# Performance work log

Measured on AMD Instinct MI355X. Metric: run time of the kernel, lower is better.

The kernel has to match this reference:

```python
import jax, jax.numpy as jnp
import numpy as np

FI_BIT, FI_GROUP = 8, 64
FW_BIT, FW_GROUP = 8, 64


def quantize_bfp(x, bit, group):
    """Block-floating-point quantize: groups of `group` elems along the last dim
    share the exponent of the group max; mantissas are rounded to `bit` bits."""
    shp = x.shape
    xg = x.reshape(shp[:-1] + (shp[-1] // group, group))
    maxabs = jnp.max(jnp.abs(xg), axis=-1, keepdims=True)
    e = jnp.floor(jnp.log2(jnp.maximum(maxabs, jnp.asarray(1e-38, x.dtype))))
    step = jnp.exp2(e - (bit - 1))  # quantization step for shared exponent e
    qmax = 2 ** (bit - 1) - 1
    q = jnp.clip(jnp.round(xg / step), -(qmax + 1), qmax) * step
    q = jnp.where(maxabs == 0, jnp.zeros_like(q), q)
    return q.reshape(shp)


def setup_inputs() -> dict:
    key = jax.random.key(0)
    k1, k2, k3 = jax.random.split(key, 3)
    N, IN, OUT = 4096, 4096, 4096
    x = jax.random.normal(k1, (N, IN), dtype=jnp.float32)
    # weight/bias initialized uniform(-0.1, 0.1) as in the torch module
    weight = jax.random.uniform(k2, (OUT, IN), dtype=jnp.float32, minval=-0.1, maxval=0.1)
    bias = jax.random.uniform(k3, (OUT,), dtype=jnp.float32, minval=-0.1, maxval=0.1)
    return {"x": x, "weight": weight, "bias": bias}


def reference(x, weight, bias):
    xq = quantize_bfp(x, FI_BIT, FI_GROUP)          # [N, IN]
    wq = quantize_bfp(weight, FW_BIT, FW_GROUP)     # [OUT, IN]
    out = jnp.einsum('ni,oi->no', xq, wq)
    # Faithful to the original forward: F.linear adds bias once, then the
    # explicit `output += bias` adds it a second time.
    out = out + 2.0 * bias[None, :]
    return out
```

## Files before the change

### kernel.cpp

```cpp
#include <hip/hip_runtime.h>
#include <stdint.h>

typedef __bf16 bf16_t;
typedef __attribute__((ext_vector_type(8))) __bf16 bf16x8;
typedef __attribute__((ext_vector_type(4))) float f32x4;

#define NDIM 4096

__global__ __launch_bounds__(256) void quant_bfp(const float* __restrict__ in0,
                                                 bf16_t* __restrict__ out0,
                                                 const float* __restrict__ in1,
                                                 bf16_t* __restrict__ out1) {
    const float* in = blockIdx.y ? in1 : in0;
    bf16_t* out     = blockIdx.y ? out1 : out0;
    const int t = blockIdx.x * 256 + threadIdx.x;
    float4 a = ((const float4*)in)[2 * t];
    float4 b = ((const float4*)in)[2 * t + 1];
    float m = fmaxf(fmaxf(fmaxf(fabsf(a.x), fabsf(a.y)), fmaxf(fabsf(a.z), fabsf(a.w))),
                    fmaxf(fmaxf(fabsf(b.x), fabsf(b.y)), fmaxf(fabsf(b.z), fabsf(b.w))));
    m = fmaxf(m, __shfl_xor(m, 1));
    m = fmaxf(m, __shfl_xor(m, 2));
    m = fmaxf(m, __shfl_xor(m, 4));
    const int e = (int)((__float_as_uint(m) >> 23) & 0xFF) - 127;
    float step = __uint_as_float((uint32_t)(e + 120) << 23);
    float inv  = __uint_as_float((uint32_t)(134 - e) << 23);
    if (m == 0.0f) { step = 0.0f; inv = 0.0f; }
    float q[8] = {a.x, a.y, a.z, a.w, b.x, b.y, b.z, b.w};
    union { bf16_t h[8]; uint4 u; } o;
#pragma unroll
    for (int i = 0; i < 8; ++i)
        o.h[i] = (bf16_t)(fminf(fmaxf(rintf(q[i] * inv), -128.0f), 127.0f) * step);
    ((uint4*)out)[t] = o.u;
}

__device__ __forceinline__ void g2l16(const bf16_t* g, void* l) {
    __builtin_amdgcn_global_load_lds(
        (__attribute__((address_space(1))) void*)g,
        (__attribute__((address_space(3))) void*)l, 16, 0, 0);
}

__global__ __launch_bounds__(256) void gemm_bfp(const bf16_t* __restrict__ A,
                                                const bf16_t* __restrict__ B,
                                                const float* __restrict__ bias,
                                                float* __restrict__ C) {
    __shared__ bf16_t sA[128 * 64];
    __shared__ bf16_t sB[128 * 64];

    const int tid  = threadIdx.x;
    const int wave = tid >> 6;
    const int lane = tid & 63;

    const int p  = blockIdx.y * 32 + blockIdx.x;
    const int bn = ((p & 7) << 2) | ((p >> 3) & 3);
    const int bm = p >> 5;

    const int m_wave = (wave >> 1) * 64;
    const int n_wave = (wave & 1) * 64;

    const int srow = tid >> 3;
    const int swz  = (((tid & 7) ^ (srow & 7)) * 8);

    const bf16_t* pA[4];
    const bf16_t* pB[4];
#pragma unroll
    for (int i = 0; i < 4; ++i) {
        pA[i] = A + (size_t)(bm * 128 + i * 32 + srow) * NDIM + swz;
        pB[i] = B + (size_t)(bn * 128 + i * 32 + srow) * NDIM + swz;
    }

    f32x4 acc[4][4];
#pragma unroll
    for (int i = 0; i < 4; ++i)
#pragma unroll
        for (int j = 0; j < 4; ++j)
            acc[i][j] = (f32x4){0.0f, 0.0f, 0.0f, 0.0f};

    const int quad = lane >> 4;
    const int l16  = lane & 15;
    const int rsw  = l16 & 7;
    const int ce0  = (quad ^ rsw) * 8;
    const int ce1  = ((4 + quad) ^ rsw) * 8;

    for (int kt = 0; kt < NDIM; kt += 64) {
#pragma unroll
        for (int i = 0; i < 4; ++i) {
            g2l16(pA[i], (char*)sA + i * 4096 + tid * 16);
            pA[i] += 64;
        }
#pragma unroll
        for (int i = 0; i < 4; ++i) {
            g2l16(pB[i], (char*)sB + i * 4096 + tid * 16);
            pB[i] += 64;
        }
        __syncthreads();

#pragma unroll
        for (int ks = 0; ks < 64; ks += 32) {
            const int ce = ks ? ce1 : ce0;
            bf16x8 af[4], bfr[4];
#pragma unroll
            for (int i = 0; i < 4; ++i)
                af[i] = *(const bf16x8*)&sA[(m_wave + i * 16 + l16) * 64 + ce];
#pragma unroll
            for (int j = 0; j < 4; ++j)
                bfr[j] = *(const bf16x8*)&sB[(n_wave + j * 16 + l16) * 64 + ce];
#pragma unroll
            for (int i = 0; i < 4; ++i)
#pragma unroll
                for (int j = 0; j < 4; ++j)
                    acc[i][j] = __builtin_amdgcn_mfma_f32_16x16x32_bf16(
                        af[i], bfr[j], acc[i][j], 0, 0, 0);
        }
        __syncthreads();
    }

    const int row0 = bm * 128 + m_wave + quad * 4;
    const int col0 = bn * 128 + n_wave + l16;
#pragma unroll
    for (int j = 0; j < 4; ++j) {
        const int c = col0 + j * 16;
        const float bv = 2.0f * bias[c];
#pragma unroll
        for (int i = 0; i < 4; ++i) {
            const int r = row0 + i * 16;
#pragma unroll
            for (int reg = 0; reg < 4; ++reg)
                C[(size_t)(r + reg) * NDIM + c] = acc[i][j][reg] + bv;
        }
    }
}

extern "C" void kernel_launch(void* const* d_in, const int* in_sizes, int n_in,
                              void* d_out, int out_size, void* d_ws, size_t ws_size,
                              hipStream_t stream) {
    const float* x    = (const float*)d_in[0];
    const float* w    = (const float*)d_in[1];
    const float* bias = (const float*)d_in[2];
    float* out = (float*)d_out;

    bf16_t* xq = (bf16_t*)d_ws;
    bf16_t* wq = xq + (size_t)NDIM * NDIM;

    const int qblocks = (NDIM * NDIM / 8) / 256;
    dim3 qgrid(qblocks, 2);
    quant_bfp<<<qgrid, 256, 0, stream>>>(x, xq, w, wq);

    dim3 grid(NDIM / 128, NDIM / 128);
    gemm_bfp<<<grid, 256, 0, stream>>>(xq, wq, bias, out);
}
```

Baseline: 300.5 us.

## Prefetch next K-tile into registers while computing on current LDS tile

Replaces the direct global-to-LDS loads with register staging: the next K-tile is loaded from global memory into registers before the MFMA loop runs, then written to LDS at the start of the next iteration. This is meant to overlap global memory latency with matrix compute, which the previous load-sync-compute sequence serialized. It costs extra VGPRs for the staging buffers and an explicit LDS store pass, and there is still a single LDS buffer guarded by two barriers per iteration.

```diff
diff --git a/kernel.cpp b/kernel.cpp
--- a/kernel.cpp
+++ b/kernel.cpp
@@ -33,12 +33,6 @@
     ((uint4*)out)[t] = o.u;
 }
 
-__device__ __forceinline__ void g2l16(const bf16_t* g, void* l) {
-    __builtin_amdgcn_global_load_lds(
-        (__attribute__((address_space(1))) void*)g,
-        (__attribute__((address_space(3))) void*)l, 16, 0, 0);
-}
-
 __global__ __launch_bounds__(256) void gemm_bfp(const bf16_t* __restrict__ A,
                                                 const bf16_t* __restrict__ B,
                                                 const float* __restrict__ bias,
@@ -60,13 +54,15 @@
     const int srow = tid >> 3;
     const int swz  = (((tid & 7) ^ (srow & 7)) * 8);
 
-    const bf16_t* pA[4];
-    const bf16_t* pB[4];
+    const uint4* pA[4];
+    const uint4* pB[4];
 #pragma unroll
     for (int i = 0; i < 4; ++i) {
-        pA[i] = A + (size_t)(bm * 128 + i * 32 + srow) * NDIM + swz;
-        pB[i] = B + (size_t)(bn * 128 + i * 32 + srow) * NDIM + swz;
+        pA[i] = (const uint4*)(A + (size_t)(bm * 128 + i * 32 + srow) * NDIM + swz);
+        pB[i] = (const uint4*)(B + (size_t)(bn * 128 + i * 32 + srow) * NDIM + swz);
     }
+    uint4* wA = (uint4*)((char*)sA + tid * 16);
+    uint4* wB = (uint4*)((char*)sB + tid * 16);
 
     f32x4 acc[4][4];
 #pragma unroll
@@ -81,18 +77,26 @@
     const int ce0  = (quad ^ rsw) * 8;
     const int ce1  = ((4 + quad) ^ rsw) * 8;
 
+    uint4 rA[4], rB[4];
+#pragma unroll
+    for (int i = 0; i < 4; ++i) { rA[i] = *pA[i]; pA[i] += 8; }
+#pragma unroll
+    for (int i = 0; i < 4; ++i) { rB[i] = *pB[i]; pB[i] += 8; }
+
     for (int kt = 0; kt < NDIM; kt += 64) {
+        if (kt) __syncthreads();
 #pragma unroll
-        for (int i = 0; i < 4; ++i) {
-            g2l16(pA[i], (char*)sA + i * 4096 + tid * 16);
-            pA[i] += 64;
+        for (int i = 0; i < 4; ++i) wA[i * 256] = rA[i];
+#pragma unroll
+        for (int i = 0; i < 4; ++i) wB[i * 256] = rB[i];
+        __syncthreads();
+
+        if (kt + 64 < NDIM) {
+#pragma unroll
+            for (int i = 0; i < 4; ++i) { rA[i] = *pA[i]; pA[i] += 8; }
+#pragma unroll
+            for (int i = 0; i < 4; ++i) { rB[i] = *pB[i]; pB[i] += 8; }
         }
-#pragma unroll
-        for (int i = 0; i < 4; ++i) {
-            g2l16(pB[i], (char*)sB + i * 4096 + tid * 16);
-            pB[i] += 64;
-        }
-        __syncthreads();
 
 #pragma unroll
         for (int ks = 0; ks < 64; ks += 32) {
@@ -111,7 +115,6 @@
                     acc[i][j] = __builtin_amdgcn_mfma_f32_16x16x32_bf16(
                         af[i], bfr[j], acc[i][j], 0, 0, 0);
         }
-        __syncthreads();
     }
 
     const int row0 = bm * 128 + m_wave + quad * 4;
```

Result: slower. 712.7 us (+137.2%).
